# Performance work log

Hardware: AMD Instinct MI355X
Metric: run time of the kernel (lower is better)

## Reference

```python
import jax, jax.numpy as jnp
import numpy as np

N, D, K = 32768, 512, 4096  # flattened tokens, latent dim, codebook size


def setup_inputs() -> dict:
    key = jax.random.key(0)
    k1, k2 = jax.random.split(key)
    z_e = jax.random.normal(k1, (N, D), dtype=jnp.float32)
    codebook = jax.random.normal(k2, (K, D), dtype=jnp.float32)
    return {"z_e": z_e, "codebook": codebook, "is_train": 1}


def reference(z_e, codebook, is_train):
    # torch.cdist(z_e, codebook) -> argmin over codes. sqrt is monotone, so
    # argmin of squared distance is identical; use the expansion
    # ||a-b||^2 = ||a||^2 - 2 a.b + ||b||^2 for a single GEMM.
    z_sq = jnp.sum(z_e * z_e, axis=1, keepdims=True)            # [N,1]
    c_sq = jnp.sum(codebook * codebook, axis=1)[None, :]        # [1,K]
    dist2 = z_sq - 2.0 * jnp.einsum('nd,kd->nk', z_e, codebook) + c_sq  # [N,K]
    encoding_indices = jnp.argmin(dist2, axis=1)                # [N]

    # codebook usage frequency (scatter-add of ones)
    codebook_freq = jnp.zeros((K,), dtype=jnp.float32).at[encoding_indices].add(1.0)

    # one-hot matmul quantization (== gather codebook[indices])
    encodings = jax.nn.one_hot(encoding_indices, K, dtype=codebook.dtype)  # [N,K]
    z_q = jnp.matmul(encodings, codebook)                       # [N,D]

    # straight-through estimator when training
    z_q_ste = z_e + jax.lax.stop_gradient(z_q - z_e)
    z_q = jnp.where(jnp.asarray(is_train, dtype=bool), z_q_ste, z_q)
    return z_q, encoding_indices, codebook_freq
```

## Files before the change

### kernel.cpp

```cpp
#include <hip/hip_runtime.h>
#include <float.h>
#include <stdint.h>
#include <stddef.h>

#define D_DIM 512
#define MARGIN 1.5f

typedef unsigned short ushort_t;
typedef unsigned int u32;
typedef __attribute__((ext_vector_type(8))) short short8v;
typedef __attribute__((ext_vector_type(8))) unsigned short ushort8v;
typedef __attribute__((ext_vector_type(4))) float f32x4;

__device__ __forceinline__ ushort_t f32_bf16_rne(float x) {
    u32 u = __float_as_uint(x);
    u32 r = (u + 0x7fffu + ((u >> 16) & 1u)) >> 16;
    return (ushort_t)r;
}
__device__ __forceinline__ void gload_lds16(const void* g, void* l) {
    __builtin_amdgcn_global_load_lds(
        (const __attribute__((address_space(1))) u32*)(g),
        (__attribute__((address_space(3))) u32*)(l), 16, 0, 0);
}

__global__ __launch_bounds__(256) void split_z_kernel(const float* __restrict__ z,
                                                      ushort_t* __restrict__ z_hi,
                                                      long total8) {
    long i = (long)blockIdx.x * 256 + threadIdx.x;
    if (i >= total8) return;
    const float4* p = (const float4*)(z + i * 8);
    float4 a = p[0], b = p[1];
    float x[8] = {a.x, a.y, a.z, a.w, b.x, b.y, b.z, b.w};
    ushort8v h;
    #pragma unroll
    for (int j = 0; j < 8; ++j) h[j] = f32_bf16_rne(x[j]);
    *(ushort8v*)(z_hi + i * 8) = h;
}

__global__ __launch_bounds__(256) void split_cb_kernel(const float* __restrict__ cb,
                                                       ushort_t* __restrict__ cb_hi,
                                                       float* __restrict__ csq32,
                                                       double* __restrict__ csq64,
                                                       float* __restrict__ freq,
                                                       int K) {
    int tid = threadIdx.x;
    int gt = blockIdx.x * 256 + tid;
    if (gt < K) freq[gt] = 0.0f;

    int wv = tid >> 6, lane = tid & 63;
    int k = blockIdx.x * 4 + wv;
    if (k >= K) return;
    const float* row = cb + (size_t)k * D_DIM;
    float4 a = *(const float4*)(row + lane * 8);
    float4 b = *(const float4*)(row + lane * 8 + 4);
    float x[8] = {a.x, a.y, a.z, a.w, b.x, b.y, b.z, b.w};
    ushort8v h;
    double s = 0.0;
    #pragma unroll
    for (int j = 0; j < 8; ++j) {
        s += (double)x[j] * x[j];
        h[j] = f32_bf16_rne(x[j]);
    }
    *(ushort8v*)(cb_hi + (size_t)k * D_DIM + lane * 8) = h;
    #pragma unroll
    for (int off = 32; off > 0; off >>= 1) s += __shfl_down(s, off);
    if (lane == 0) { csq64[k] = s; csq32[k] = (float)s; }
}

__global__ __launch_bounds__(512, 2) void pass1_mfma_kernel(
        const ushort_t* __restrict__ z_hi, const ushort_t* __restrict__ cb_hi,
        const float* __restrict__ csq32,
        float* __restrict__ cm_v0, int* __restrict__ cm_cnt,
        u32* __restrict__ cm_mask,
        float* __restrict__ cand_v, int* __restrict__ cand_k, int K) {
    extern __shared__ char smem[];
    const int tid = threadIdx.x;
    const int wid = tid >> 6;
    const int lane = tid & 63;
    const int wm = wid >> 1, wn = wid & 1;
    const int c = lane & 15, g = lane >> 4;
    const int row0 = blockIdx.x * 256;
    const int half = blockIdx.y;

    u32 stgA[4], stgB[2];
    #pragma unroll
    for (int r = 0; r < 4; ++r) {
        int s = r * 512 + tid, rw = s >> 3, p = s & 7;
        stgA[r] = (u32)(rw * 1024 + ((p ^ (rw & 7)) << 4));
    }
    #pragma unroll
    for (int r = 0; r < 2; ++r) {
        int s = r * 512 + tid, rw = s >> 3, p = s & 7;
        stgB[r] = (u32)(rw * 1024 + ((p ^ (rw & 7)) << 4));
    }
    u32 rdA[2][4], rdB[2][4];
    #pragma unroll
    for (int f = 0; f < 4; ++f) {
        int rl = wm * 64 + f * 16 + c;
        rdA[0][f] = (u32)(rl * 128 + ((g ^ (rl & 7)) << 4));
        rdA[1][f] = rdA[0][f] ^ 64u;
        int cl = wn * 64 + f * 16 + c;
        rdB[0][f] = (u32)(cl * 128 + ((g ^ (cl & 7)) << 4));
        rdB[1][f] = rdB[0][f] ^ 64u;
    }

    const char* pA = (const char*)z_hi + (size_t)row0 * 1024;
    const char* pB = (const char*)cb_hi + (size_t)half * 2048 * 1024;

    const ptrdiff_t eA7 = -896;
    const ptrdiff_t eB7 = 131072 - 896;

    f32x4 acc[4][4];
    float tv0[16], tv1[16]; int tk0[16];
    #pragma unroll
    for (int i = 0; i < 16; ++i) { tv0[i] = FLT_MAX; tv1[i] = FLT_MAX; tk0[i] = 0; }

    auto STAGE = [&](int buf) {
        char* base = smem + buf * 49152;
        #pragma unroll
        for (int r = 0; r < 4; ++r)
            gload_lds16(pA + stgA[r], base + r * 8192 + wid * 1024);
        #pragma unroll
        for (int r = 0; r < 2; ++r)
            gload_lds16(pB + stgB[r], base + 32768 + r * 8192 + wid * 1024);
    };
    auto COMPUTE = [&](int buf) {
        const char* Abase = smem + buf * 49152;
        const char* Bb = Abase + 32768;
        #pragma unroll
        for (int ks = 0; ks < 2; ++ks) {
            short8v a[4], b[4];
            #pragma unroll
            for (int f = 0; f < 4; ++f) a[f] = *(const short8v*)(Abase + rdA[ks][f]);
            #pragma unroll
            for (int f = 0; f < 4; ++f) b[f] = *(const short8v*)(Bb + rdB[ks][f]);
            #pragma unroll
            for (int fm = 0; fm < 4; ++fm)
                #pragma unroll
                for (int fn = 0; fn < 4; ++fn)
                    acc[fm][fn] = __builtin_amdgcn_mfma_f32_16x16x32_bf16(
                        a[fm], b[fn], acc[fm][fn], 0, 0, 0);
        }
    };
    auto BARA = [&]() {
        __builtin_amdgcn_s_barrier();
        __builtin_amdgcn_sched_barrier(0);
    };
    auto WAITBARB = [&]() {
        asm volatile("s_waitcnt vmcnt(6)" ::: "memory");
        __builtin_amdgcn_s_barrier();
        __builtin_amdgcn_sched_barrier(0);
    };

    STAGE(0); pA += 128; pB += 128;

    #pragma unroll 1
    for (int ci = 0; ci < 16; ++ci) {
        int code0 = (half * 16 + ci) << 7;
        float cq[4];
        #pragma unroll
        for (int fn = 0; fn < 4; ++fn) cq[fn] = csq32[code0 + wn * 64 + fn * 16 + c];

        f32x4 zz = {0.f, 0.f, 0.f, 0.f};
        #pragma unroll
        for (int fm = 0; fm < 4; ++fm)
            #pragma unroll
            for (int fn = 0; fn < 4; ++fn) acc[fm][fn] = zz;

        #pragma unroll 1
        for (int tp = 0; tp < 4; ++tp) {
            BARA();
            STAGE(1);
            { ptrdiff_t dA = 128, dB = 128;
              if (tp == 3) { dA = eA7; dB = eB7; }
              pA += dA; pB += dB; }
            WAITBARB();
            COMPUTE(0);
            BARA();
            STAGE(0);
            pA += 128; pB += 128;
            WAITBARB();
            COMPUTE(1);
        }

        #pragma unroll
        for (int fm = 0; fm < 4; ++fm)
            #pragma unroll
            for (int fn = 0; fn < 4; ++fn) {
                int code = code0 + wn * 64 + fn * 16 + c;
                #pragma unroll
                for (int rg = 0; rg < 4; ++rg) {
                    int rp = fm * 4 + rg;
                    float sv = fmaf(-2.0f, acc[fm][fn][rg], cq[fn]);
                    bool b0 = sv < tv0[rp];
                    bool b1 = sv < tv1[rp];
                    tv1[rp] = b0 ? tv0[rp] : (b1 ? sv : tv1[rp]);
                    tv0[rp] = b0 ? sv : tv0[rp];
                    tk0[rp] = b0 ? code : tk0[rp];
                }
            }
    }

    __syncthreads();
    float* mv = (float*)smem;
    int*   mi = (int*)(smem + 65536);
    #pragma unroll
    for (int fm = 0; fm < 4; ++fm)
        #pragma unroll
        for (int rg = 0; rg < 4; ++rg) {
            int rl = wm * 64 + fm * 16 + g * 4 + rg;
            int slot = wn * 16 + c;
            int rp = fm * 4 + rg;
            mv[rl * 64 + slot * 2]     = tv0[rp];
            mv[rl * 64 + slot * 2 + 1] = tv1[rp];
            mi[rl * 32 + slot]         = tk0[rp];
        }
    __syncthreads();
    if (tid < 256) {
        const float* rv = mv + tid * 64;
        const int*   ri = mi + tid * 32;
        float v0 = FLT_MAX;
        #pragma unroll 8
        for (int j = 0; j < 32; ++j) v0 = fminf(v0, rv[2 * j]);
        float lim = v0 + MARGIN;
        u32 mask = 0;
        int cnt = 0; int ks[8]; float vs[8];
        for (int j = 0; j < 32; ++j) {
            if (rv[2 * j] <= lim) {
                if (cnt < 8) { ks[cnt] = ri[j]; vs[cnt] = rv[2 * j]; cnt++; }
                else mask |= 1u << j;
            }
            if (rv[2 * j + 1] <= lim) mask |= 1u << j;
        }
        int gidx = (row0 + tid) * 2 + half;
        cm_v0[gidx]  = v0;
        cm_cnt[gidx] = cnt;
        cm_mask[gidx] = mask;
        for (int m = 0; m < cnt; ++m) {
            cand_v[(size_t)gidx * 8 + m] = vs[m];
            cand_k[(size_t)gidx * 8 + m] = ks[m];
        }
    }
}

__global__ __launch_bounds__(256) void pass2_new_kernel(
        const float* __restrict__ z, const float* __restrict__ cb,
        const double* __restrict__ csq64,
        const float* __restrict__ cm_v0, const int* __restrict__ cm_cnt,
        const u32* __restrict__ cm_mask,
        const float* __restrict__ cand_v, const int* __restrict__ cand_k,
        float* __restrict__ zq, float* __restrict__ oidx, float* __restrict__ freq,
        int N, int K) {
    int lane = threadIdx.x & 63;
    int row = blockIdx.x * 4 + (threadIdx.x >> 6);
    if (row >= N) return;
    const int Khalf = K >> 1;

    float v0a = cm_v0[row * 2], v0b = cm_v0[row * 2 + 1];
    int   na  = cm_cnt[row * 2], nb = cm_cnt[row * 2 + 1];
    u32   ma  = cm_mask[row * 2], mb = cm_mask[row * 2 + 1];
    float lim = fminf(v0a, v0b) + MARGIN;
    if (na > 8 || na < 0) { na = 0; ma = 0xffffffffu; }
    if (nb > 8 || nb < 0) { nb = 0; mb = 0xffffffffu; }

    int ks[16]; int cnt = 0;
    {
        for (int m = 0; m < na; ++m) {
            size_t idx = (size_t)(row * 2) * 8 + m;
            if (cand_v[idx] <= lim) ks[cnt++] = cand_k[idx];
        }
        for (int m = 0; m < nb; ++m) {
            size_t idx = (size_t)(row * 2 + 1) * 8 + m;
            if (cand_v[idx] <= lim) ks[cnt++] = cand_k[idx];
        }
    }

    int best_k;
    if (cnt == 1 && ma == 0 && mb == 0) {
        best_k = ks[0];
    } else {
        const float* zrow = z + (size_t)row * D_DIM;
        double best_s = DBL_MAX; int bk = 0x7fffffff;

        {
            float4 z0 = *(const float4*)(zrow + lane * 4);
            float4 z1 = *(const float4*)(zrow + 256 + lane * 4);
            for (int m = 0; m < cnt; ++m) {
                int k = ks[m];
                const float* crow = cb + (size_t)k * D_DIM;
                float4 c0 = *(const float4*)(crow + lane * 4);
                float4 c1 = *(const float4*)(crow + 256 + lane * 4);
                double a = (double)z0.x * c0.x + (double)z0.y * c0.y +
                           (double)z0.z * c0.z + (double)z0.w * c0.w +
                           (double)z1.x * c1.x + (double)z1.y * c1.y +
                           (double)z1.z * c1.z + (double)z1.w * c1.w;
                #pragma unroll
                for (int off = 32; off > 0; off >>= 1) a += __shfl_down(a, off);
                if (lane == 0) {
                    double s = csq64[k] - 2.0 * a;
                    if (s < best_s || (s == best_s && k < bk)) { best_s = s; bk = k; }
                }
            }
            best_s = __shfl(best_s, 0);
            bk     = __shfl(bk, 0);
        }

        if (ma | mb) {
            const int cs = lane >> 3;
            const int ds = lane & 7;
            const float* zch = zrow + ds * 64;
            float4 zr[16];
            #pragma unroll
            for (int j = 0; j < 16; ++j) zr[j] = *(const float4*)(zch + j * 4);

            double bs2 = DBL_MAX; int bk2 = 0x7fffffff;
            for (int h = 0; h < 2; ++h) {
                u32 m = h ? mb : ma;
                while (m) {
                    int s = __ffs(m) - 1; m &= m - 1;
                    for (int tb = 0; tb < 8; ++tb) {
                        int t = tb * 8 + cs;
                        int code = h * Khalf + ((t >> 2) << 7) + ((s >> 4) << 6)
                                 + ((t & 3) << 4) + (s & 15);
                        const float* crow = cb + (size_t)code * D_DIM + ds * 64;
                        double a0 = 0.0, a1 = 0.0, a2 = 0.0, a3 = 0.0;
                        #pragma unroll
                        for (int j = 0; j < 16; j += 4) {
                            float4 c0 = *(const float4*)(crow + j * 4);
                            float4 c1 = *(const float4*)(crow + j * 4 + 4);
                            float4 c2 = *(const float4*)(crow + j * 4 + 8);
                            float4 c3 = *(const float4*)(crow + j * 4 + 12);
                            a0 += (double)zr[j].x * c0.x + (double)zr[j].y * c0.y +
                                  (double)zr[j].z * c0.z + (double)zr[j].w * c0.w;
                            a1 += (double)zr[j+1].x * c1.x + (double)zr[j+1].y * c1.y +
                                  (double)zr[j+1].z * c1.z + (double)zr[j+1].w * c1.w;
                            a2 += (double)zr[j+2].x * c2.x + (double)zr[j+2].y * c2.y +
                                  (double)zr[j+2].z * c2.z + (double)zr[j+2].w * c2.w;
                            a3 += (double)zr[j+3].x * c3.x + (double)zr[j+3].y * c3.y +
                                  (double)zr[j+3].z * c3.z + (double)zr[j+3].w * c3.w;
                        }
                        double a = (a0 + a1) + (a2 + a3);
                        #pragma unroll
                        for (int off = 1; off < 8; off <<= 1) a += __shfl_xor(a, off);
                        double sc = csq64[code] - 2.0 * a;
                        if (sc < bs2 || (sc == bs2 && code < bk2)) { bs2 = sc; bk2 = code; }
                    }
                }
            }
            #pragma unroll
            for (int off = 32; off > 0; off >>= 1) {
                double os = __shfl_down(bs2, off);
                int    ok2 = __shfl_down(bk2, off);
                if (os < bs2 || (os == bs2 && ok2 < bk2)) { bs2 = os; bk2 = ok2; }
            }
            bs2 = __shfl(bs2, 0);
            bk2 = __shfl(bk2, 0);
            if (bs2 < best_s || (bs2 == best_s && bk2 < bk)) { best_s = bs2; bk = bk2; }
        }
        best_k = bk;
    }

    if (lane == 0) {
        oidx[row] = (float)best_k;
        atomicAdd(&freq[best_k], 1.0f);
    }
    const float* crow = cb + (size_t)best_k * D_DIM;
    *(float4*)(zq + (size_t)row * D_DIM + lane * 4) = *(const float4*)(crow + lane * 4);
    *(float4*)(zq + (size_t)row * D_DIM + 256 + lane * 4) = *(const float4*)(crow + 256 + lane * 4);
}

__global__ __launch_bounds__(256) void csq_kernel(const float* __restrict__ cb,
                                                  float* __restrict__ csq32,
                                                  double* __restrict__ csq64,
                                                  float* __restrict__ freq,
                                                  int K) {
    int tid = threadIdx.x;
    int gt = blockIdx.x * 256 + tid;
    if (gt < K) freq[gt] = 0.0f;
    int wave = tid >> 6, lane = tid & 63;
    int k = blockIdx.x * 4 + wave;
    if (k >= K) return;
    const float* row = cb + (size_t)k * D_DIM;
    float4 v0 = *(const float4*)(row + lane * 4);
    float4 v1 = *(const float4*)(row + 256 + lane * 4);
    double s = (double)v0.x * v0.x + (double)v0.y * v0.y +
               (double)v0.z * v0.z + (double)v0.w * v0.w +
               (double)v1.x * v1.x + (double)v1.y * v1.y +
               (double)v1.z * v1.z + (double)v1.w * v1.w;
    #pragma unroll
    for (int off = 32; off > 0; off >>= 1) s += __shfl_down(s, off);
    if (lane == 0) { csq64[k] = s; csq32[k] = (float)s; }
}

__device__ __forceinline__ void top4_insert(float (&v)[4], int (&ki)[4], float s, int k) {
    if (s < v[3]) {
        v[3] = s; ki[3] = k;
        if (v[3] < v[2]) {
            float t = v[3]; v[3] = v[2]; v[2] = t; int u = ki[3]; ki[3] = ki[2]; ki[2] = u;
            if (v[2] < v[1]) {
                t = v[2]; v[2] = v[1]; v[1] = t; u = ki[2]; ki[2] = ki[1]; ki[1] = u;
                if (v[1] < v[0]) {
                    t = v[1]; v[1] = v[0]; v[0] = t; u = ki[1]; ki[1] = ki[0]; ki[0] = u;
                }
            }
        }
    }
}

#define BM 64
#define BK 128
#define BD 32
#define ZS_STRIDE (BM + 4)
#define CS_STRIDE (BK + 4)

__global__ __launch_bounds__(256) void pass1_kernel(const float* __restrict__ z,
                                                    const float* __restrict__ cb,
                                                    const float* __restrict__ csq32,
                                                    float* __restrict__ cand_v,
                                                    int* __restrict__ cand_i,
                                                    int K) {
    __shared__ float zs[BD][ZS_STRIDE];
    __shared__ float cs[BD][CS_STRIDE];
    __shared__ float mvv[BM][64];
    __shared__ int   mii[BM][64];
    const int tid = threadIdx.x;
    const int rg = tid & 15;
    const int cg = tid >> 4;
    const int row0 = blockIdx.x * BM;
    float tv[4][4]; int tk[4][4];
    #pragma unroll
    for (int r = 0; r < 4; ++r)
        #pragma unroll
        for (int m = 0; m < 4; ++m) { tv[r][m] = FLT_MAX; tk[r][m] = 0x7fffffff; }
    for (int kt = 0; kt < K; kt += BK) {
        float acc[4][8];
        #pragma unroll
        for (int r = 0; r < 4; ++r)
            #pragma unroll
            for (int cc = 0; cc < 8; ++cc) acc[r][cc] = 0.0f;
        for (int dt = 0; dt < D_DIM; dt += BD) {
            __syncthreads();
            #pragma unroll
            for (int i = 0; i < 2; ++i) {
                int lin = tid + i * 256;
                int zr = lin >> 3, dg = lin & 7;
                float4 v = *(const float4*)(z + (size_t)(row0 + zr) * D_DIM + dt + dg * 4);
                zs[dg * 4 + 0][zr] = v.x; zs[dg * 4 + 1][zr] = v.y;
                zs[dg * 4 + 2][zr] = v.z; zs[dg * 4 + 3][zr] = v.w;
            }
            #pragma unroll
            for (int i = 0; i < 4; ++i) {
                int lin = tid + i * 256;
                int cr = lin >> 3, dg = lin & 7;
                float4 v = *(const float4*)(cb + (size_t)(kt + cr) * D_DIM + dt + dg * 4);
                cs[dg * 4 + 0][cr] = v.x; cs[dg * 4 + 1][cr] = v.y;
                cs[dg * 4 + 2][cr] = v.z; cs[dg * 4 + 3][cr] = v.w;
            }
            __syncthreads();
            #pragma unroll
            for (int d = 0; d < BD; ++d) {
                float4 a = *(const float4*)&zs[d][rg * 4];
                float4 b0 = *(const float4*)&cs[d][cg * 8];
                float4 b1 = *(const float4*)&cs[d][cg * 8 + 4];
                float av[4] = {a.x, a.y, a.z, a.w};
                float bv[8] = {b0.x, b0.y, b0.z, b0.w, b1.x, b1.y, b1.z, b1.w};
                #pragma unroll
                for (int r = 0; r < 4; ++r)
                    #pragma unroll
                    for (int cc = 0; cc < 8; ++cc)
                        acc[r][cc] = fmaf(av[r], bv[cc], acc[r][cc]);
            }
        }
        #pragma unroll
        for (int cc = 0; cc < 8; ++cc) {
            int k = kt + cg * 8 + cc;
            float cq = csq32[k];
            #pragma unroll
            for (int r = 0; r < 4; ++r) {
                float s = fmaf(-2.0f, acc[r][cc], cq);
                top4_insert(tv[r], tk[r], s, k);
            }
        }
    }
    __syncthreads();
    #pragma unroll
    for (int r = 0; r < 4; ++r)
        #pragma unroll
        for (int m = 0; m < 4; ++m) {
            mvv[rg * 4 + r][cg * 4 + m] = tv[r][m];
            mii[rg * 4 + r][cg * 4 + m] = tk[r][m];
        }
    __syncthreads();
    if (tid < BM) {
        int row = tid;
        float bv[4] = {FLT_MAX, FLT_MAX, FLT_MAX, FLT_MAX};
        int   bk[4] = {0x7fffffff, 0x7fffffff, 0x7fffffff, 0x7fffffff};
        for (int j = 0; j < 64; ++j) top4_insert(bv, bk, mvv[row][j], mii[row][j]);
        #pragma unroll
        for (int m = 0; m < 4; ++m) {
            cand_v[(size_t)(row0 + row) * 4 + m] = bv[m];
            cand_i[(size_t)(row0 + row) * 4 + m] = bk[m];
        }
    }
}

__global__ __launch_bounds__(256) void pass2_kernel(const float* __restrict__ z,
                                                    const float* __restrict__ cb,
                                                    const double* __restrict__ csq64,
                                                    const float* __restrict__ cand_v,
                                                    const int* __restrict__ cand_i,
                                                    float* __restrict__ zq,
                                                    float* __restrict__ oidx,
                                                    float* __restrict__ freq,
                                                    int N, int K) {
    int lane = threadIdx.x & 63;
    int row = blockIdx.x * 4 + (threadIdx.x >> 6);
    if (row >= N) return;
    const float* zrow = z + (size_t)row * D_DIM;
    float4 z0 = *(const float4*)(zrow + lane * 4);
    float4 z1 = *(const float4*)(zrow + 256 + lane * 4);
    float cv0 = cand_v[(size_t)row * 4 + 0];
    float cv3 = cand_v[(size_t)row * 4 + 3];
    int ci[4];
    bool ok = (cv3 - cv0 >= 0.1f);
    #pragma unroll
    for (int m = 0; m < 4; ++m) {
        ci[m] = cand_i[(size_t)row * 4 + m];
        if (ci[m] < 0 || ci[m] >= K) ok = false;
    }
    double best_s = DBL_MAX;
    int best_k = 0;
    if (ok) {
        #pragma unroll
        for (int m = 0; m < 4; ++m) {
            int k = ci[m];
            const float* crow = cb + (size_t)k * D_DIM;
            float4 c0 = *(const float4*)(crow + lane * 4);
            float4 c1 = *(const float4*)(crow + 256 + lane * 4);
            double a = (double)z0.x * c0.x + (double)z0.y * c0.y +
                       (double)z0.z * c0.z + (double)z0.w * c0.w +
                       (double)z1.x * c1.x + (double)z1.y * c1.y +
                       (double)z1.z * c1.z + (double)z1.w * c1.w;
            #pragma unroll
            for (int off = 32; off > 0; off >>= 1) a += __shfl_down(a, off);
            if (lane == 0) {
                double s = csq64[k] - 2.0 * a;
                if (s < best_s || (s == best_s && k < best_k)) { best_s = s; best_k = k; }
            }
        }
    } else {
        for (int k = 0; k < K; ++k) {
            const float* crow = cb + (size_t)k * D_DIM;
            float4 c0 = *(const float4*)(crow + lane * 4);
            float4 c1 = *(const float4*)(crow + 256 + lane * 4);
            double a = (double)z0.x * c0.x + (double)z0.y * c0.y +
                       (double)z0.z * c0.z + (double)z0.w * c0.w +
                       (double)z1.x * c1.x + (double)z1.y * c1.y +
                       (double)z1.z * c1.z + (double)z1.w * c1.w;
            #pragma unroll
            for (int off = 32; off > 0; off >>= 1) a += __shfl_down(a, off);
            if (lane == 0) {
                double s = csq64[k] - 2.0 * a;
                if (s < best_s) { best_s = s; best_k = k; }
            }
        }
    }
    best_k = __shfl(best_k, 0);
    if (lane == 0) {
        oidx[row] = (float)best_k;
        atomicAdd(&freq[best_k], 1.0f);
    }
    const float* crow = cb + (size_t)best_k * D_DIM;
    *(float4*)(zq + (size_t)row * D_DIM + lane * 4) = *(const float4*)(crow + lane * 4);
    *(float4*)(zq + (size_t)row * D_DIM + 256 + lane * 4) = *(const float4*)(crow + 256 + lane * 4);
}

extern "C" void kernel_launch(void* const* d_in, const int* in_sizes, int n_in,
                              void* d_out, int out_size, void* d_ws, size_t ws_size,
                              hipStream_t stream) {
    const float* z  = (const float*)d_in[0];
    const float* cb = (const float*)d_in[1];
    const int N = in_sizes[0] / D_DIM;
    const int K = in_sizes[1] / D_DIM;

    float* zq   = (float*)d_out;
    float* oidx = zq + (size_t)N * D_DIM;
    float* freq = oidx + N;

    char* ws = (char*)d_ws;
    size_t o = 0;
    ushort_t* z_hi  = (ushort_t*)(ws + o); o += (size_t)N * D_DIM * 2;
    ushort_t* cbh   = (ushort_t*)(ws + o); o += (size_t)K * D_DIM * 2;
    o = (o + 255) & ~(size_t)255;
    float*  csq32   = (float*)(ws + o);    o += (size_t)K * sizeof(float);
    o = (o + 255) & ~(size_t)255;
    double* csq64   = (double*)(ws + o);   o += (size_t)K * sizeof(double);
    o = (o + 255) & ~(size_t)255;
    float* cm_v0    = (float*)(ws + o);    o += (size_t)N * 2 * sizeof(float);
    int*   cm_cnt   = (int*)(ws + o);      o += (size_t)N * 2 * sizeof(int);
    u32*   cm_mask  = (u32*)(ws + o);      o += (size_t)N * 2 * sizeof(u32);
    float* cand_vv  = (float*)(ws + o);    o += (size_t)N * 2 * 8 * sizeof(float);
    int*   cand_kk  = (int*)(ws + o);      o += (size_t)N * 2 * 8 * sizeof(int);
    size_t needed = o + 262144;

    if (ws_size >= needed && (N % 256) == 0 && K == 4096) {
        hipFuncSetAttribute((const void*)pass1_mfma_kernel,
                            hipFuncAttributeMaxDynamicSharedMemorySize, 98304);
        long total8 = (long)N * D_DIM / 8;
        hipLaunchKernelGGL(split_z_kernel, dim3((unsigned)((total8 + 255) / 256)), dim3(256),
                           0, stream, z, z_hi, total8);
        hipLaunchKernelGGL(split_cb_kernel, dim3(K / 4), dim3(256), 0, stream,
                           cb, cbh, csq32, csq64, freq, K);
        hipLaunchKernelGGL(pass1_mfma_kernel, dim3(N / 256, 2), dim3(512), 98304, stream,
                           z_hi, cbh, csq32, cm_v0, cm_cnt, cm_mask, cand_vv, cand_kk, K);
        hipLaunchKernelGGL(pass2_new_kernel, dim3(N / 4), dim3(256), 0, stream,
                           z, cb, csq64, cm_v0, cm_cnt, cm_mask, cand_vv, cand_kk,
                           zq, oidx, freq, N, K);
    } else {
        size_t o2 = 0;
        float*  f_csq32 = (float*)(ws + o2);  o2 += (size_t)K * sizeof(float);
        o2 = (o2 + 255) & ~(size_t)255;
        double* f_csq64 = (double*)(ws + o2); o2 += (size_t)K * sizeof(double);
        o2 = (o2 + 255) & ~(size_t)255;
        float*  cand_v  = (float*)(ws + o2);  o2 += (size_t)N * 4 * sizeof(float);
        int*    cand_i  = (int*)(ws + o2);
        hipLaunchKernelGGL(csq_kernel, dim3((K + 3) / 4), dim3(256), 0, stream,
                           cb, f_csq32, f_csq64, freq, K);
        hipLaunchKernelGGL(pass1_kernel, dim3(N / BM), dim3(256), 0, stream,
                           z, cb, f_csq32, cand_v, cand_i, K);
        hipLaunchKernelGGL(pass2_kernel, dim3(N / 4), dim3(256), 0, stream,
                           z, cb, f_csq64, cand_v, cand_i, zq, oidx, freq, N, K);
    }
}
```

Baseline: 246.9 us.

## Triple-buffer LDS staging in pass1 MFMA loop with one barrier per step

The pass1 GEMM main loop moves from a two-buffer LDS ping-pong with two barriers per k-step to a rotating three-buffer scheme. Each step issues the next tile's global-to-LDS loads into a free buffer, waits on the older loads and takes a single barrier, then computes. The goal is to halve barrier stalls and give loads more time to land before they are consumed. In exchange, dynamic LDS per block grows from 96 KB to 144 KB, which rules out any extra block per CU and depends on the barrier ordering being enough to avoid overwriting a buffer still being read.

```diff
diff --git a/kernel.cpp b/kernel.cpp
--- a/kernel.cpp
+++ b/kernel.cpp
@@ -115,8 +115,8 @@
     #pragma unroll
     for (int i = 0; i < 16; ++i) { tv0[i] = FLT_MAX; tv1[i] = FLT_MAX; tk0[i] = 0; }
 
-    auto STAGE = [&](int buf) {
-        char* base = smem + buf * 49152;
+    auto STAGE = [&](u32 off) {
+        char* base = smem + off;
         #pragma unroll
         for (int r = 0; r < 4; ++r)
             gload_lds16(pA + stgA[r], base + r * 8192 + wid * 1024);
@@ -124,8 +124,8 @@
         for (int r = 0; r < 2; ++r)
             gload_lds16(pB + stgB[r], base + 32768 + r * 8192 + wid * 1024);
     };
-    auto COMPUTE = [&](int buf) {
-        const char* Abase = smem + buf * 49152;
+    auto COMPUTE = [&](u32 off) {
+        const char* Abase = smem + off;
         const char* Bb = Abase + 32768;
         #pragma unroll
         for (int ks = 0; ks < 2; ++ks) {
@@ -142,17 +142,15 @@
                         a[fm], b[fn], acc[fm][fn], 0, 0, 0);
         }
     };
-    auto BARA = [&]() {
-        __builtin_amdgcn_s_barrier();
-        __builtin_amdgcn_sched_barrier(0);
-    };
-    auto WAITBARB = [&]() {
+    auto WAITBAR = [&]() {
         asm volatile("s_waitcnt vmcnt(6)" ::: "memory");
         __builtin_amdgcn_s_barrier();
         __builtin_amdgcn_sched_barrier(0);
     };
 
     STAGE(0); pA += 128; pB += 128;
+    u32 offS = 49152;
+    u32 offC = 0;
 
     #pragma unroll 1
     for (int ci = 0; ci < 16; ++ci) {
@@ -168,19 +166,15 @@
             for (int fn = 0; fn < 4; ++fn) acc[fm][fn] = zz;
 
         #pragma unroll 1
-        for (int tp = 0; tp < 4; ++tp) {
-            BARA();
-            STAGE(1);
+        for (int t = 0; t < 8; ++t) {
+            STAGE(offS);
             { ptrdiff_t dA = 128, dB = 128;
-              if (tp == 3) { dA = eA7; dB = eB7; }
+              if (t == 6) { dA = eA7; dB = eB7; }
               pA += dA; pB += dB; }
-            WAITBARB();
-            COMPUTE(0);
-            BARA();
-            STAGE(0);
-            pA += 128; pB += 128;
-            WAITBARB();
-            COMPUTE(1);
+            WAITBAR();
+            COMPUTE(offC);
+            offS = (offS == 98304u) ? 0u : offS + 49152u;
+            offC = (offC == 98304u) ? 0u : offC + 49152u;
         }
 
         #pragma unroll
@@ -605,13 +599,13 @@
 
     if (ws_size >= needed && (N % 256) == 0 && K == 4096) {
         hipFuncSetAttribute((const void*)pass1_mfma_kernel,
-                            hipFuncAttributeMaxDynamicSharedMemorySize, 98304);
+                            hipFuncAttributeMaxDynamicSharedMemorySize, 147456);
         long total8 = (long)N * D_DIM / 8;
         hipLaunchKernelGGL(split_z_kernel, dim3((unsigned)((total8 + 255) / 256)), dim3(256),
                            0, stream, z, z_hi, total8);
         hipLaunchKernelGGL(split_cb_kernel, dim3(K / 4), dim3(256), 0, stream,
                            cb, cbh, csq32, csq64, freq, K);
-        hipLaunchKernelGGL(pass1_mfma_kernel, dim3(N / 256, 2), dim3(512), 98304, stream,
+        hipLaunchKernelGGL(pass1_mfma_kernel, dim3(N / 256, 2), dim3(512), 147456, stream,
                            z_hi, cbh, csq32, cm_v0, cm_cnt, cm_mask, cand_vv, cand_kk, K);
         hipLaunchKernelGGL(pass2_new_kernel, dim3(N / 4), dim3(256), 0, stream,
                            z, cb, csq64, cm_v0, cm_cnt, cm_mask, cand_vv, cand_kk,
```

New measurement: 240.1 us. -2.8%, faster.
